# Kernel tuning notes

Measured on AMD Instinct MI355X. Metric: run time of the kernel, lower is better.

Reference implementation:

```python
import jax, jax.numpy as jnp
import numpy as np

G = 40   # voxel grid size (forward hardcodes bounds 0..39)
P = 16   # max points stored per voxel
K = 32   # n_neighbor
B = 4
N = 65536
S = 4096


def setup_inputs() -> dict:
    key = jax.random.key(0)
    kp, kc = jax.random.split(key)
    pos = jax.random.uniform(kp, (B, N, 3), dtype=jnp.float32)          # points in [0,1)
    centroids = jax.random.randint(kc, (B, S), 0, N, dtype=jnp.int32)   # sampled centroid indices
    # Build the voxel hash table (tensorized version of index_voxels dict) on host.
    pos_np = np.asarray(pos)
    vid = (pos_np * (G - 1)).astype(np.int32)                            # [B,N,3], ids in 0..38
    flat = (vid[..., 0] * G + vid[..., 1]) * G + vid[..., 2]             # [B,N]
    vp = np.zeros((B, G * G * G, P), dtype=np.int32)
    cnt = np.zeros((B, G * G * G), dtype=np.int32)
    for b in range(B):
        order = np.argsort(flat[b], kind='stable')
        sf = flat[b][order]
        rank = np.arange(N) - np.searchsorted(sf, sf, side='left')       # slot within voxel
        keep = rank < P
        vp[b, sf[keep], rank[keep]] = order[keep]
        cnt[b] = np.minimum(np.bincount(flat[b], minlength=G * G * G), P)
    voxel_points = vp.reshape(B, G, G, G, P)
    voxel_counts = cnt.reshape(B, G, G, G)
    mask = (voxel_counts > 0).astype(np.int32)                            # occupied-voxel mask
    # 27-neighborhood voxel list, as the module receives it precomputed.
    off = np.stack(np.meshgrid(*[np.arange(-1, 2)] * 3, indexing='ij'), -1).reshape(27, 3)
    coords = np.stack(np.meshgrid(*[np.arange(G)] * 3, indexing='ij'), -1)  # [G,G,G,3]
    nb = coords[:, :, :, None, :] + off[None, None, None]                   # [G,G,G,27,3]
    neighbour_voxel_list = np.broadcast_to(nb, (B, G, G, G, 27, 3)).astype(np.int32).copy()
    return {
        'pos': pos,
        'centroids': centroids,
        'voxel_points': jnp.asarray(voxel_points),
        'voxel_counts': jnp.asarray(voxel_counts),
        'neighbour_voxel_list': jnp.asarray(neighbour_voxel_list),
        'mask': jnp.asarray(mask),
        'voxel_size': G,
    }


def reference(pos, centroids, voxel_points, voxel_counts, neighbour_voxel_list, mask, voxel_size):
    Bs, Ss = centroids.shape
    hi = voxel_size - 1                                   # bounds check 0..39
    # index_points(pos, centroids)
    center_pos = jnp.take_along_axis(pos, centroids[:, :, None].astype(jnp.int32), axis=1)  # [B,S,3]
    cvid = (center_pos * (voxel_size - 1)).astype(jnp.int32)                                # [B,S,3]
    bI = jnp.arange(Bs)[:, None, None]                    # [B,1,1]
    # neighbour voxels of each centroid's voxel: [B,S,27,3]
    nb = neighbour_voxel_list[jnp.arange(Bs)[:, None], cvid[..., 0], cvid[..., 1], cvid[..., 2]]
    nx, ny, nz = nb[..., 0], nb[..., 1], nb[..., 2]       # each [B,S,27]
    in_bounds = (nx >= 0) & (nx <= hi) & (ny >= 0) & (ny <= hi) & (nz >= 0) & (nz <= hi)
    nxc = jnp.clip(nx, 0, hi); nyc = jnp.clip(ny, 0, hi); nzc = jnp.clip(nz, 0, hi)
    vvalid = in_bounds & (mask[bI, nxc, nyc, nzc] > 0)    # skip out-of-bounds / empty voxels
    cand = voxel_points[bI, nxc, nyc, nzc]                # [B,S,27,P] candidate point indices
    cnts = voxel_counts[bI, nxc, nyc, nzc]                # [B,S,27]
    valid = vvalid[..., None] & (jnp.arange(P)[None, None, None, :] < cnts[..., None])
    C = 27 * P
    cand = cand.reshape(Bs, Ss, C)
    valid = valid.reshape(Bs, Ss, C)
    # take the first K valid candidates per centroid (deterministic stand-in for random.sample)
    order = jnp.cumsum(valid, axis=-1) - 1                # running index among valid candidates
    dest = jnp.where(valid & (order < K), order, K)       # invalid / overflow -> dump slot K
    out = jnp.repeat(centroids[:, :, None].astype(jnp.int32), K + 1, axis=2)  # pad = centroid idx
    out = out.at[bI, jnp.arange(Ss)[None, :, None], dest].set(cand)
    return out[:, :, :K].astype(jnp.float32)              # [B,S,K] group_idx, float like original
```

## Files before the change

kernel.cpp:

```cpp
#include <hip/hip_runtime.h>

constexpr int Gc = 40;
constexpr int Pc = 16;
constexpr int Kc = 32;
constexpr int Bc = 4;
constexpr int Nc = 65536;
constexpr int Sc = 4096;

__global__ __launch_bounds__(256) void frnn_kernel(
    const float* __restrict__ pos,
    const int*   __restrict__ centroids,
    const int*   __restrict__ voxel_points,
    const int*   __restrict__ voxel_counts,
    float*       __restrict__ out)
{
    const int tid  = blockIdx.x * 256 + threadIdx.x;
    const int g    = tid >> 5;
    const int lane = threadIdx.x & 31;
    const int b    = g >> 12;
    const int c    = centroids[g];

    const float* pp = pos + ((size_t)b * Nc + (size_t)c) * 3;
    const int vx = (int)(pp[0] * 39.0f);
    const int vy = (int)(pp[1] * 39.0f);
    const int vz = (int)(pp[2] * 39.0f);

    const int* vcnt_b = voxel_counts + (size_t)b * (Gc * Gc * Gc);
    const int* vpts_b = voxel_points + (size_t)b * (Gc * Gc * Gc) * Pc;

    int cnt = 0, cell = 0;
    if (lane < 27) {
        int dx = lane / 9 - 1;
        int dy = (lane / 3) % 3 - 1;
        int dz = lane % 3 - 1;
        int nx = vx + dx, ny = vy + dy, nz = vz + dz;
        if ((unsigned)nx < (unsigned)Gc && (unsigned)ny < (unsigned)Gc &&
            (unsigned)nz < (unsigned)Gc) {
            cell = (nx * Gc + ny) * Gc + nz;
            cnt  = vcnt_b[cell];
            if (cnt > Pc) cnt = Pc;
        }
    }

    int incl = cnt;
    #pragma unroll
    for (int off = 1; off < 32; off <<= 1) {
        int n = __shfl_up(incl, off, 32);
        if (lane >= off) incl += n;
    }
    const int excl  = incl - cnt;
    const int total = __shfl(incl, 31, 32);

    int v = 0;
    #pragma unroll
    for (int s = 16; s; s >>= 1) {
        int t = __shfl(incl, v + s - 1, 32);
        v += (t <= lane) ? s : 0;
    }
    const int excl_v = __shfl(excl, v & 31, 32);
    const int cell_v = __shfl(cell, v & 31, 32);
    const int j      = lane - excl_v;
    const int idx    = cell_v * Pc + j;

    const int  tk    = total < Kc ? total : Kc;
    const bool valid = lane < tk;
    const int  sidx  = valid ? idx : 0;
    const float pv   = (float)vpts_b[sidx];
    out[(size_t)g * Kc + lane] = valid ? pv : (float)c;
}

extern "C" void kernel_launch(void* const* d_in, const int* in_sizes, int n_in,
                              void* d_out, int out_size, void* d_ws, size_t ws_size,
                              hipStream_t stream) {
    const float* pos       = (const float*)d_in[0];
    const int*   centroids = (const int*)d_in[1];
    const int*   vpts      = (const int*)d_in[2];
    const int*   vcnt      = (const int*)d_in[3];
    float* out = (float*)d_out;

    const int total_threads = Bc * Sc * 32;
    const int block = 256;
    const int grid  = total_threads / block;
    frnn_kernel<<<grid, block, 0, stream>>>(pos, centroids, vpts, vcnt, out);
}
```

Before: 131.0 us.

## Remap blocks per XCD by batch and prefetch first voxel slots with counts

Block indices are remapped so each pair of XCDs handles one batch, which is meant to keep that batch's voxel tables in the L2 of those XCDs. Each neighbour lane now loads the first four point indices of its voxel as an int4 alongside the count. These are shuffled to consumer lanes, so most outputs avoid a dependent second gather. Lanes whose slot is past index 3 still issue a scattered load. Out-of-bounds lanes now read cell 0 unconditionally, which adds some wasted traffic.

Measured after the change: 133.6 us. About the same (+2.0%).

```diff
diff --git a/kernel.cpp b/kernel.cpp
--- a/kernel.cpp
+++ b/kernel.cpp
@@ -14,11 +14,15 @@
     const int*   __restrict__ voxel_counts,
     float*       __restrict__ out)
 {
-    const int tid  = blockIdx.x * 256 + threadIdx.x;
-    const int g    = tid >> 5;
+    const int i    = blockIdx.x;
+    const int xcd  = i & 7;
+    const int b    = xcd >> 1;
+    const int wb   = (i >> 3) * 2 + (xcd & 1);
+    const int gin  = wb * 8 + (threadIdx.x >> 5);
+    const int g    = b * Sc + gin;
     const int lane = threadIdx.x & 31;
-    const int b    = g >> 12;
-    const int c    = centroids[g];
+
+    const int c = centroids[g];
 
     const float* pp = pos + ((size_t)b * Nc + (size_t)c) * 3;
     const int vx = (int)(pp[0] * 39.0f);
@@ -29,17 +33,19 @@
     const int* vpts_b = voxel_points + (size_t)b * (Gc * Gc * Gc) * Pc;
 
     int cnt = 0, cell = 0;
+    int4 pre = make_int4(0, 0, 0, 0);
     if (lane < 27) {
         int dx = lane / 9 - 1;
         int dy = (lane / 3) % 3 - 1;
         int dz = lane % 3 - 1;
         int nx = vx + dx, ny = vy + dy, nz = vz + dz;
-        if ((unsigned)nx < (unsigned)Gc && (unsigned)ny < (unsigned)Gc &&
-            (unsigned)nz < (unsigned)Gc) {
-            cell = (nx * Gc + ny) * Gc + nz;
-            cnt  = vcnt_b[cell];
-            if (cnt > Pc) cnt = Pc;
-        }
+        const bool inb = (unsigned)nx < (unsigned)Gc &&
+                         (unsigned)ny < (unsigned)Gc &&
+                         (unsigned)nz < (unsigned)Gc;
+        cell = inb ? (nx * Gc + ny) * Gc + nz : 0;
+        int cr = vcnt_b[cell];
+        pre = *reinterpret_cast<const int4*>(vpts_b + (size_t)cell * Pc);
+        cnt = inb ? (cr > Pc ? Pc : cr) : 0;
     }
 
     int incl = cnt;
@@ -57,16 +63,24 @@
         int t = __shfl(incl, v + s - 1, 32);
         v += (t <= lane) ? s : 0;
     }
-    const int excl_v = __shfl(excl, v & 31, 32);
-    const int cell_v = __shfl(cell, v & 31, 32);
+    const int vm     = v & 31;
+    const int excl_v = __shfl(excl, vm, 32);
+    const int cell_v = __shfl(cell, vm, 32);
+    const int q0     = __shfl(pre.x, vm, 32);
+    const int q1     = __shfl(pre.y, vm, 32);
+    const int q2     = __shfl(pre.z, vm, 32);
+    const int q3     = __shfl(pre.w, vm, 32);
     const int j      = lane - excl_v;
-    const int idx    = cell_v * Pc + j;
 
     const int  tk    = total < Kc ? total : Kc;
     const bool valid = lane < tk;
-    const int  sidx  = valid ? idx : 0;
-    const float pv   = (float)vpts_b[sidx];
-    out[(size_t)g * Kc + lane] = valid ? pv : (float)c;
+
+    int pv = (j == 1) ? q1 : (j == 2) ? q2 : (j == 3) ? q3 : q0;
+    if (valid && j > 3) {
+        pv = vpts_b[cell_v * Pc + j];
+    }
+
+    out[(size_t)g * Kc + lane] = valid ? (float)pv : (float)c;
 }
 
 extern "C" void kernel_launch(void* const* d_in, const int* in_sizes, int n_in,
```
